# Kernel optimization log

Measured on AMD Instinct MI355X. Metric: run time of the kernel, lower is better.

Reference implementation:

```python
import jax, jax.numpy as jnp
import numpy as np

S, B, D, E2 = 2048, 32, 1024, 1024  # src_len, batch, dec_hid_dim, 2*enc_hid_dim


def setup_inputs() -> dict:
    key = jax.random.key(0)
    k1, k2, k3, k4, k5 = jax.random.split(key, 5)
    scale = 1.0 / np.sqrt(D)
    return {
        "dec_prev_hidden": jax.random.normal(k1, (B, D), dtype=jnp.float32),
        "enc_outputs": jax.random.normal(k2, (S, B, E2), dtype=jnp.float32),
        "Wb": jax.random.normal(k3, (D, D), dtype=jnp.float32) * scale,
        "Wc": jax.random.normal(k4, (D, E2), dtype=jnp.float32) * scale,
        "Wa": jax.random.normal(k5, (D,), dtype=jnp.float32) * scale,
    }


def reference(dec_prev_hidden, enc_outputs, Wb, Wc, Wa):
    # weighted_s_t_1: [B, D] broadcast over seq axis; weighted_H: [S, B, D]
    weighted_s = jnp.einsum('bd,ed->be', dec_prev_hidden, Wb)          # [B, D]
    weighted_H = jnp.einsum('sbe,de->sbd', enc_outputs, Wc)            # [S, B, D]
    score = jnp.einsum('sbd,d->sb', jnp.tanh(weighted_H + weighted_s), Wa)  # [S, B]
    # torch F.softmax with no dim on a 3-D tensor -> dim=0 (seq axis)
    attn = jax.nn.softmax(score, axis=0)                               # [S, B]
    # bmm([B,1,S], [B,S,2E]) -> [B,1,2E], then permute -> [1,B,2E]
    context = jnp.einsum('sb,sbe->be', attn, enc_outputs)              # [B, 2E]
    return context[None, :, :]                                         # [1, B, 2E]
```

## Files before the change

### kernel.cpp

```cpp
#include <hip/hip_runtime.h>
#include <hip/hip_bf16.h>
#include <stdint.h>

#define S_LEN 2048
#define BATCH 32
#define MROWS (S_LEN*BATCH)

typedef __attribute__((ext_vector_type(8))) short bf16x8;
typedef __attribute__((ext_vector_type(4))) float f32x4;
typedef unsigned short ushort_t;

__device__ inline unsigned int pk2bf(float a, float b) {
  float2 t; t.x = a; t.y = b;
  __hip_bfloat162 h = __float22bfloat162_rn(t);
  union { __hip_bfloat162 h; unsigned int u; } c; c.h = h;
  return c.u;
}

__device__ inline float bflo(unsigned int u) { return __uint_as_float(u << 16); }
__device__ inline float bfhi(unsigned int u) { return __uint_as_float(u & 0xffff0000u); }

__device__ inline void gload_lds16(const void* g, void* l) {
  __builtin_amdgcn_global_load_lds(
      (const __attribute__((address_space(1))) unsigned int*)g,
      (__attribute__((address_space(3))) unsigned int*)l, 16, 0, 0);
}

__device__ inline float fast_tanh(float x) {
  float e = __expf(2.0f * x);
  return 1.0f - 2.0f / (e + 1.0f);
}

__global__ __launch_bounds__(256) void prep_small_kernel(
    const float* __restrict__ dec, const float* __restrict__ Wb,
    const float* __restrict__ Wc, ushort_t* __restrict__ WcBf,
    float* __restrict__ wsum)
{
  const int t = threadIdx.x;
  const int bid = blockIdx.x;
  if (bid < 64) {
    const int base = bid * 16384;
    for (int i = 0; i < 16; ++i) {
      int idx = base + i * 1024 + t * 4;
      float4 v = *(const float4*)(Wc + idx);
      uint2 w; w.x = pk2bf(v.x, v.y); w.y = pk2bf(v.z, v.w);
      *(uint2*)(WcBf + idx) = w;
    }
  } else {
    const int j = bid - 64;
    __shared__ float sdec[32][65];
    __shared__ float swb[32][65];
    const int b = t & 31, nl = t >> 5;
    float acc0 = 0.f, acc1 = 0.f, acc2 = 0.f, acc3 = 0.f;
    for (int c = 0; c < 16; ++c) {
      __syncthreads();
      for (int idx = t; idx < 2048; idx += 256) {
        int rr = idx >> 6, dd = idx & 63;
        sdec[rr][dd] = dec[rr * 1024 + c * 64 + dd];
        swb[rr][dd]  = Wb[(size_t)(j * 32 + rr) * 1024 + c * 64 + dd];
      }
      __syncthreads();
      #pragma unroll 8
      for (int dd = 0; dd < 64; ++dd) {
        float dv = sdec[b][dd];
        acc0 += dv * swb[nl][dd];
        acc1 += dv * swb[nl + 8][dd];
        acc2 += dv * swb[nl + 16][dd];
        acc3 += dv * swb[nl + 24][dd];
      }
    }
    wsum[b * 1024 + j * 32 + nl]      = acc0;
    wsum[b * 1024 + j * 32 + nl + 8]  = acc1;
    wsum[b * 1024 + j * 32 + nl + 16] = acc2;
    wsum[b * 1024 + j * 32 + nl + 24] = acc3;
  }
}

__global__ __launch_bounds__(256, 4) void score_kernel(
    const float4* __restrict__ encF4, ushort_t* __restrict__ encBf,
    const ushort_t* __restrict__ WcBf, const float* __restrict__ wsum,
    const float* __restrict__ Wa, float* __restrict__ scoreP8)
{
  __shared__ ushort_t Ab[128][64];
  __shared__ ushort_t Bb[128][64];
  __shared__ float scorep[128];

  const int tid = threadIdx.x;
  const int lane = tid & 63;
  const int l15 = lane & 15, q = lane >> 4;
  const int r7 = l15 & 7;
  const int wid = tid >> 6;
  const int wr = wid >> 1, wc = wid & 1;
  const int bid = blockIdx.x;
  const int mi = bid & 15, nblk = (bid >> 4) & 7, mg = bid >> 7;
  const size_t rowBase = (size_t)(mg * 16 + mi) * 128;

  if (tid < 128) scorep[tid] = 0.f;

  const int tRow = tid >> 4;
  const int f4 = tid & 15;
  const int swzT = (((f4 >> 1) ^ (tRow & 7)) * 8) + ((f4 & 1) * 4);

  int bOff[4], dOff[4];
  #pragma unroll
  for (int k = 0; k < 4; ++k) {
    const int s = k * 256 + tid;
    const int r = s >> 3, c = s & 7;
    bOff[k] = (int)((nblk * 128 + r) * 1024 + ((c ^ (r & 7)) * 8));
    dOff[k] = s * 8;
  }
  ushort_t* const aL = &Ab[0][0];
  ushort_t* const bL = &Bb[0][0];

  int aRow[4], bRow[4];
  #pragma unroll
  for (int m = 0; m < 4; ++m) aRow[m] = (wr * 64 + m * 16 + l15) * 64;
  #pragma unroll
  for (int n = 0; n < 4; ++n) bRow[n] = (wc * 64 + n * 16 + l15) * 64;
  const int ch0 = (q ^ r7) * 8;
  const int ch1 = ((4 + q) ^ r7) * 8;

  f32x4 acc[4][4];
  #pragma unroll
  for (int m = 0; m < 4; ++m)
    #pragma unroll
    for (int n = 0; n < 4; ++n) { f32x4 z = {0.f,0.f,0.f,0.f}; acc[m][n] = z; }

  for (int kt = 0; kt < 16; ++kt) {
    const int ko = kt * 64;
    #pragma unroll
    for (int k = 0; k < 4; ++k)
      gload_lds16(WcBf + ko + bOff[k], bL + dOff[k]);

    float4 av[8];
    #pragma unroll
    for (int k = 0; k < 8; ++k)
      av[k] = encF4[(rowBase + k * 16 + tRow) * 256 + kt * 16 + f4];

    #pragma unroll
    for (int k = 0; k < 8; ++k) {
      uint2 w;
      w.x = pk2bf(av[k].x, av[k].y);
      w.y = pk2bf(av[k].z, av[k].w);
      const int r = k * 16 + tRow;
      *(uint2*)(aL + r * 64 + swzT) = w;
      if (nblk == 0)
        *(uint2*)(encBf + (rowBase + r) * 1024 + ko + f4 * 4) = w;
    }
    __syncthreads();

    #pragma unroll
    for (int kk = 0; kk < 2; ++kk) {
      const int cho = kk ? ch1 : ch0;
      bf16x8 af[4], bv[4];
      #pragma unroll
      for (int m = 0; m < 4; ++m) af[m] = *(const bf16x8*)(aL + aRow[m] + cho);
      #pragma unroll
      for (int n = 0; n < 4; ++n) bv[n] = *(const bf16x8*)(bL + bRow[n] + cho);
      #pragma unroll
      for (int m = 0; m < 4; ++m)
        #pragma unroll
        for (int n = 0; n < 4; ++n)
          acc[m][n] = __builtin_amdgcn_mfma_f32_16x16x32_bf16(
              af[m], bv[n], acc[m][n], 0, 0, 0);
    }
    __syncthreads();
  }

  #pragma unroll
  for (int m = 0; m < 4; ++m) {
    #pragma unroll
    for (int i = 0; i < 4; ++i) {
      const int rowl = wr * 64 + m * 16 + q * 4 + i;
      const int bb2 = rowl & 31;
      float v = 0.f;
      #pragma unroll
      for (int n = 0; n < 4; ++n) {
        const int col = nblk * 128 + wc * 64 + n * 16 + l15;
        float x = acc[m][n][i] + wsum[bb2 * 1024 + col];
        v += fast_tanh(x) * Wa[col];
      }
      v += __shfl_xor(v, 1); v += __shfl_xor(v, 2);
      v += __shfl_xor(v, 4); v += __shfl_xor(v, 8);
      if (l15 == 0) atomicAdd(&scorep[rowl], v);
    }
  }
  __syncthreads();
  if (tid < 128) scoreP8[(rowBase + tid) * 8 + nblk] = scorep[tid];
}

__global__ __launch_bounds__(256) void ctx_kernel(
    const ushort_t* __restrict__ encBf, const float* __restrict__ scoreP8,
    float* __restrict__ out)
{
  const int b = blockIdx.x & 31, sc = blockIdx.x >> 5;
  const int t = threadIdx.x;
  __shared__ float eCh[128];
  __shared__ float red[256];

  const int chunk0 = sc * 128;
  float ssum = 0.f;
  for (int s = t; s < S_LEN; s += 256) {
    const float4* p = (const float4*)(scoreP8 + ((size_t)s * 32 + b) * 8);
    float4 u = p[0], v = p[1];
    float scv = ((u.x + u.y) + (u.z + u.w)) + ((v.x + v.y) + (v.z + v.w));
    float e = __expf(scv);
    ssum += e;
    const int d = s - chunk0;
    if ((unsigned)d < 128u) eCh[d] = e;
  }
  red[t] = ssum;
  __syncthreads();
  #pragma unroll
  for (int o = 128; o > 0; o >>= 1) {
    if (t < o) red[t] += red[t + o];
    __syncthreads();
  }
  const float inv = 1.0f / red[0];

  float a0 = 0.f, a1 = 0.f, a2 = 0.f, a3 = 0.f;
  const int e0 = t * 4;
  #pragma unroll 4
  for (int si = 0; si < 128; ++si) {
    const int s = chunk0 + si;
    const float a = eCh[si];
    uint2 w = *(const uint2*)(encBf + ((size_t)s * 32 + b) * 1024 + e0);
    a0 += a * bflo(w.x); a1 += a * bfhi(w.x);
    a2 += a * bflo(w.y); a3 += a * bfhi(w.y);
  }
  float* op = out + b * 1024 + e0;
  atomicAdd(op + 0, a0 * inv); atomicAdd(op + 1, a1 * inv);
  atomicAdd(op + 2, a2 * inv); atomicAdd(op + 3, a3 * inv);
}

extern "C" void kernel_launch(void* const* d_in, const int* in_sizes, int n_in,
                              void* d_out, int out_size, void* d_ws, size_t ws_size,
                              hipStream_t stream) {
  const float* dec = (const float*)d_in[0];
  const float* enc = (const float*)d_in[1];
  const float* Wb  = (const float*)d_in[2];
  const float* Wc  = (const float*)d_in[3];
  const float* Wa  = (const float*)d_in[4];
  float* out = (float*)d_out;
  (void)in_sizes; (void)n_in; (void)ws_size;

  char* ws = (char*)d_ws;
  ushort_t* encBf   = (ushort_t*)ws;
  ushort_t* WcBf    = (ushort_t*)(ws + 134217728);
  float*    wsum    = (float*)(ws + 134217728 + 2097152);
  float*    scoreP8 = (float*)(ws + 134217728 + 2097152 + 131072);

  hipMemsetAsync(out, 0, (size_t)out_size * sizeof(float), stream);
  prep_small_kernel<<<96, 256, 0, stream>>>(dec, Wb, Wc, WcBf, wsum);
  score_kernel<<<4096, 256, 0, stream>>>((const float4*)enc, encBf, WcBf,
                                         wsum, Wa, scoreP8);
  ctx_kernel<<<512, 256, 0, stream>>>(encBf, scoreP8, out);
}
```

Baseline: 378.6 us.

## Drop bf16 encoder copy, read fp32 in ctx, prefetch next A tile in registers

```diff
diff --git a/kernel.cpp b/kernel.cpp
--- a/kernel.cpp
+++ b/kernel.cpp
@@ -16,9 +16,6 @@
   union { __hip_bfloat162 h; unsigned int u; } c; c.h = h;
   return c.u;
 }
-
-__device__ inline float bflo(unsigned int u) { return __uint_as_float(u << 16); }
-__device__ inline float bfhi(unsigned int u) { return __uint_as_float(u & 0xffff0000u); }
 
 __device__ inline void gload_lds16(const void* g, void* l) {
   __builtin_amdgcn_global_load_lds(
@@ -77,9 +74,9 @@
 }
 
 __global__ __launch_bounds__(256, 4) void score_kernel(
-    const float4* __restrict__ encF4, ushort_t* __restrict__ encBf,
-    const ushort_t* __restrict__ WcBf, const float* __restrict__ wsum,
-    const float* __restrict__ Wa, float* __restrict__ scoreP8)
+    const float4* __restrict__ encF4, const ushort_t* __restrict__ WcBf,
+    const float* __restrict__ wsum, const float* __restrict__ Wa,
+    float* __restrict__ scoreP8)
 {
   __shared__ ushort_t Ab[128][64];
   __shared__ ushort_t Bb[128][64];
@@ -100,6 +97,7 @@
   const int tRow = tid >> 4;
   const int f4 = tid & 15;
   const int swzT = (((f4 >> 1) ^ (tRow & 7)) * 8) + ((f4 & 1) * 4);
+  const float4* aTB = encF4 + (rowBase + tRow) * 256 + f4;
 
   int bOff[4], dOff[4];
   #pragma unroll
@@ -126,28 +124,34 @@
     #pragma unroll
     for (int n = 0; n < 4; ++n) { f32x4 z = {0.f,0.f,0.f,0.f}; acc[m][n] = z; }
 
+  float4 av[8];
+  #pragma unroll
+  for (int k = 0; k < 8; ++k) av[k] = aTB[k * 4096];
+
   for (int kt = 0; kt < 16; ++kt) {
+    __builtin_amdgcn_sched_barrier(0);
     const int ko = kt * 64;
     #pragma unroll
     for (int k = 0; k < 4; ++k)
       gload_lds16(WcBf + ko + bOff[k], bL + dOff[k]);
-
-    float4 av[8];
-    #pragma unroll
-    for (int k = 0; k < 8; ++k)
-      av[k] = encF4[(rowBase + k * 16 + tRow) * 256 + kt * 16 + f4];
 
     #pragma unroll
     for (int k = 0; k < 8; ++k) {
       uint2 w;
       w.x = pk2bf(av[k].x, av[k].y);
       w.y = pk2bf(av[k].z, av[k].w);
-      const int r = k * 16 + tRow;
-      *(uint2*)(aL + r * 64 + swzT) = w;
-      if (nblk == 0)
-        *(uint2*)(encBf + (rowBase + r) * 1024 + ko + f4 * 4) = w;
-    }
-    __syncthreads();
+      *(uint2*)(aL + (k * 16 + tRow) * 64 + swzT) = w;
+    }
+
+    if (kt < 15) {
+      #pragma unroll
+      for (int k = 0; k < 8; ++k) av[k] = aTB[k * 4096 + (kt + 1) * 16];
+      asm volatile("s_waitcnt vmcnt(8) lgkmcnt(0)" ::: "memory");
+    } else {
+      asm volatile("s_waitcnt vmcnt(0) lgkmcnt(0)" ::: "memory");
+    }
+    __builtin_amdgcn_s_barrier();
+    __builtin_amdgcn_sched_barrier(0);
 
     #pragma unroll
     for (int kk = 0; kk < 2; ++kk) {
@@ -164,7 +168,8 @@
           acc[m][n] = __builtin_amdgcn_mfma_f32_16x16x32_bf16(
               af[m], bv[n], acc[m][n], 0, 0, 0);
     }
-    __syncthreads();
+    __builtin_amdgcn_sched_barrier(0);
+    __builtin_amdgcn_s_barrier();
   }
 
   #pragma unroll
@@ -190,7 +195,7 @@
 }
 
 __global__ __launch_bounds__(256) void ctx_kernel(
-    const ushort_t* __restrict__ encBf, const float* __restrict__ scoreP8,
+    const float4* __restrict__ encF4, const float* __restrict__ scoreP8,
     float* __restrict__ out)
 {
   const int b = blockIdx.x & 31, sc = blockIdx.x >> 5;
@@ -219,16 +224,14 @@
   const float inv = 1.0f / red[0];
 
   float a0 = 0.f, a1 = 0.f, a2 = 0.f, a3 = 0.f;
-  const int e0 = t * 4;
   #pragma unroll 4
   for (int si = 0; si < 128; ++si) {
     const int s = chunk0 + si;
     const float a = eCh[si];
-    uint2 w = *(const uint2*)(encBf + ((size_t)s * 32 + b) * 1024 + e0);
-    a0 += a * bflo(w.x); a1 += a * bfhi(w.x);
-    a2 += a * bflo(w.y); a3 += a * bfhi(w.y);
-  }
-  float* op = out + b * 1024 + e0;
+    const float4 v = encF4[((size_t)s * 32 + b) * 256 + t];
+    a0 += a * v.x; a1 += a * v.y; a2 += a * v.z; a3 += a * v.w;
+  }
+  float* op = out + b * 1024 + t * 4;
   atomicAdd(op + 0, a0 * inv); atomicAdd(op + 1, a1 * inv);
   atomicAdd(op + 2, a2 * inv); atomicAdd(op + 3, a3 * inv);
 }
@@ -245,14 +248,13 @@
   (void)in_sizes; (void)n_in; (void)ws_size;
 
   char* ws = (char*)d_ws;
-  ushort_t* encBf   = (ushort_t*)ws;
-  ushort_t* WcBf    = (ushort_t*)(ws + 134217728);
-  float*    wsum    = (float*)(ws + 134217728 + 2097152);
-  float*    scoreP8 = (float*)(ws + 134217728 + 2097152 + 131072);
+  ushort_t* WcBf    = (ushort_t*)ws;
+  float*    wsum    = (float*)(ws + 2097152);
+  float*    scoreP8 = (float*)(ws + 2097152 + 131072);
 
   hipMemsetAsync(out, 0, (size_t)out_size * sizeof(float), stream);
   prep_small_kernel<<<96, 256, 0, stream>>>(dec, Wb, Wc, WcBf, wsum);
-  score_kernel<<<4096, 256, 0, stream>>>((const float4*)enc, encBf, WcBf,
-                                         wsum, Wa, scoreP8);
-  ctx_kernel<<<512, 256, 0, stream>>>(encBf, scoreP8, out);
-}
+  score_kernel<<<4096, 256, 0, stream>>>((const float4*)enc, WcBf, wsum, Wa,
+                                         scoreP8);
+  ctx_kernel<<<512, 256, 0, stream>>>((const float4*)enc, scoreP8, out);
+}
```

Result: slower. 460.7 us (+21.7%).
